# Kernel tuning notes

Hardware: AMD Instinct MI355X
Metric: run time of the kernel (lower is better)

The kernel has to match this reference:

```python
import jax, jax.numpy as jnp
import numpy as np

DIM = 3072
NUM_HEADS = 24
HEAD_DIM = 128
EPS = 1e-6


def setup_inputs() -> dict:
    key = jax.random.key(0)
    ks = jax.random.split(key, 16)
    B, S_new, S_cached = 2, 256, 8192
    s = 0.02
    return {
        "x": jax.random.normal(ks[0], (B, S_new, DIM), jnp.float32),
        "freqs": jax.random.uniform(ks[1], (S_new, HEAD_DIM // 2), jnp.float32, 0.0, 2 * np.pi),
        "k_cache": jax.random.normal(ks[2], (B, S_cached, DIM), jnp.float32),
        "v_cache": jax.random.normal(ks[3], (B, S_cached, DIM), jnp.float32),
        "Wq": jax.random.normal(ks[4], (DIM, DIM), jnp.float32) * s,
        "bq": jnp.zeros((DIM,), jnp.float32),
        "Wk": jax.random.normal(ks[5], (DIM, DIM), jnp.float32) * s,
        "bk": jnp.zeros((DIM,), jnp.float32),
        "Wv": jax.random.normal(ks[6], (DIM, DIM), jnp.float32) * s,
        "bv": jnp.zeros((DIM,), jnp.float32),
        "Wo": jax.random.normal(ks[7], (DIM, DIM), jnp.float32) * s,
        "bo": jnp.zeros((DIM,), jnp.float32),
        "gq": jnp.ones((DIM,), jnp.float32),
        "gk": jnp.ones((DIM,), jnp.float32),
    }


def _rmsnorm(t, g):
    return t * jax.lax.rsqrt(jnp.mean(t * t, axis=-1, keepdims=True) + EPS) * g


def _rope(t, freqs):
    # t: [B, S, DIM]; freqs: [S, HEAD_DIM//2] angles (complex e^{i*theta} multiply,
    # interleaved-pair layout, matching torch view_as_complex on (..., d//2, 2)).
    B, S, D = t.shape
    th = t.reshape(B, S, NUM_HEADS, HEAD_DIM // 2, 2)
    c = jnp.cos(freqs)[None, :, None, :]
    s = jnp.sin(freqs)[None, :, None, :]
    re = th[..., 0] * c - th[..., 1] * s
    im = th[..., 0] * s + th[..., 1] * c
    return jnp.stack([re, im], axis=-1).reshape(B, S, D)


def reference(x, freqs, k_cache, v_cache, Wq, bq, Wk, bk, Wv, bv, Wo, bo, gq, gk):
    B, S_new, _ = x.shape
    S_cached = k_cache.shape[1]
    S_tot = S_cached + S_new

    q = _rmsnorm(x @ Wq.T + bq, gq)
    k = _rmsnorm(x @ Wk.T + bk, gk)
    v = x @ Wv.T + bv

    q = _rope(q, freqs)
    k = _rope(k, freqs)

    # 'extend' cache mode: concat cached K/V with new K/V
    full_k = jnp.concatenate([k_cache, k], axis=1)
    full_v = jnp.concatenate([v_cache, v], axis=1)

    qh = q.reshape(B, S_new, NUM_HEADS, HEAD_DIM)
    kh = full_k.reshape(B, S_tot, NUM_HEADS, HEAD_DIM)
    vh = full_v.reshape(B, S_tot, NUM_HEADS, HEAD_DIM)

    scale = 1.0 / np.sqrt(HEAD_DIM)
    scores = jnp.einsum("bqhd,bkhd->bhqk", qh, kh) * scale
    probs = jax.nn.softmax(scores, axis=-1)
    out = jnp.einsum("bhqk,bkhd->bqhd", probs, vh).reshape(B, S_new, DIM)
    return out @ Wo.T + bo
```

## Files before the change

kernel.cpp:

```cpp
#include <hip/hip_runtime.h>
#include <hip/hip_bf16.h>

#define NH 24
#define HD 128
#define DM 3072
#define NB 2
#define SN 256
#define MR 512
#define SCACHE 8192
#define NCH 9

typedef float f32x4 __attribute__((ext_vector_type(4)));
typedef float f32x2 __attribute__((ext_vector_type(2)));
typedef short s16x8 __attribute__((ext_vector_type(8)));
typedef short s16x4 __attribute__((ext_vector_type(4)));
typedef unsigned u32x4 __attribute__((ext_vector_type(4)));

__device__ __forceinline__ short bfc(float f) {
    __hip_bfloat16 h = __float2bfloat16(f);
    return __builtin_bit_cast(short, h);
}

__global__ __launch_bounds__(256, 3) void gemm_bias(
    const float* __restrict__ A,
    const float* __restrict__ W0, const float* __restrict__ W1, const float* __restrict__ W2,
    const float* __restrict__ b0, const float* __restrict__ b1, const float* __restrict__ b2,
    float* __restrict__ O0, float* __restrict__ O1, float* __restrict__ O2)
{
    const int z = blockIdx.z;
    const float* W    = (z == 0) ? W0 : (z == 1) ? W1 : W2;
    const float* bias = (z == 0) ? b0 : (z == 1) ? b1 : b2;
    float* O          = (z == 0) ? O0 : (z == 1) ? O1 : O2;

    const int n0 = blockIdx.x * 128;
    const int m0 = blockIdx.y * 64;
    const int t = threadIdx.x;
    const int lane = t & 63;
    const int wave = t >> 6;
    const int l15 = lane & 15, l4 = lane >> 4;
    const int wm = (wave >> 1) * 32, wn = (wave & 1) * 64;

    __shared__ short As[64][72];
    __shared__ short Bs[128][72];

    f32x4 acc[2][4] = {};
    f32x4 areg[4], breg[8];

    #pragma unroll
    for (int i = 0; i < 4; ++i) {
        int lin = i * 256 + t;
        areg[i] = *(const f32x4*)(A + (size_t)(m0 + (lin >> 4)) * DM + (lin & 15) * 4);
    }
    #pragma unroll
    for (int i = 0; i < 8; ++i) {
        int lin = i * 256 + t;
        breg[i] = *(const f32x4*)(W + (size_t)(n0 + (lin >> 4)) * DM + (lin & 15) * 4);
    }

    for (int ks = 0; ks < DM / 64; ++ks) {
        #pragma unroll
        for (int i = 0; i < 4; ++i) {
            int lin = i * 256 + t;
            s16x4 a4;
            #pragma unroll
            for (int j = 0; j < 4; ++j) a4[j] = bfc(areg[i][j]);
            *(s16x4*)&As[lin >> 4][(lin & 15) * 4] = a4;
        }
        #pragma unroll
        for (int i = 0; i < 8; ++i) {
            int lin = i * 256 + t;
            s16x4 w4;
            #pragma unroll
            for (int j = 0; j < 4; ++j) w4[j] = bfc(breg[i][j]);
            *(s16x4*)&Bs[lin >> 4][(lin & 15) * 4] = w4;
        }
        __syncthreads();
        if (ks + 1 < DM / 64) {
            int k0 = (ks + 1) * 64;
            #pragma unroll
            for (int i = 0; i < 4; ++i) {
                int lin = i * 256 + t;
                areg[i] = *(const f32x4*)(A + (size_t)(m0 + (lin >> 4)) * DM + k0 + (lin & 15) * 4);
            }
            #pragma unroll
            for (int i = 0; i < 8; ++i) {
                int lin = i * 256 + t;
                breg[i] = *(const f32x4*)(W + (size_t)(n0 + (lin >> 4)) * DM + k0 + (lin & 15) * 4);
            }
        }
        #pragma unroll
        for (int kt = 0; kt < 2; ++kt) {
            s16x8 af[2], bfr[4];
            #pragma unroll
            for (int i = 0; i < 2; ++i)
                af[i]  = *(const s16x8*)&As[wm + i * 16 + l15][kt * 32 + l4 * 8];
            #pragma unroll
            for (int i = 0; i < 4; ++i)
                bfr[i] = *(const s16x8*)&Bs[wn + i * 16 + l15][kt * 32 + l4 * 8];
            #pragma unroll
            for (int mi = 0; mi < 2; ++mi)
                #pragma unroll
                for (int ni = 0; ni < 4; ++ni)
                    acc[mi][ni] = __builtin_amdgcn_mfma_f32_16x16x32_bf16(
                        af[mi], bfr[ni], acc[mi][ni], 0, 0, 0);
        }
        __syncthreads();
    }

    #pragma unroll
    for (int ni = 0; ni < 4; ++ni) {
        int col = n0 + wn + ni * 16 + l15;
        float bv = bias[col];
        #pragma unroll
        for (int mi = 0; mi < 2; ++mi) {
            int row = m0 + wm + mi * 16 + l4 * 4;
            #pragma unroll
            for (int r = 0; r < 4; ++r)
                O[(size_t)(row + r) * DM + col] = acc[mi][ni][r] + bv;
        }
    }
}

__global__ __launch_bounds__(256) void norm_rope(
    float* __restrict__ qf, float* __restrict__ kf, short* __restrict__ qbf,
    const float* __restrict__ gq, const float* __restrict__ gk,
    const float* __restrict__ freqs)
{
    const int buf = blockIdx.x >> 9;
    const int row = blockIdx.x & 511;
    const int t = threadIdx.x;
    float* src = buf ? kf : qf;
    const float* g = buf ? gk : gq;

    f32x2 v[6];
    float ss = 0.f;
    #pragma unroll
    for (int i = 0; i < 6; ++i) {
        int p = t + 256 * i;
        v[i] = *(const f32x2*)(src + (size_t)row * DM + 2 * p);
        ss += v[i][0] * v[i][0] + v[i][1] * v[i][1];
    }
    #pragma unroll
    for (int m = 1; m < 64; m <<= 1) ss += __shfl_xor(ss, m);
    __shared__ float red[4];
    if ((t & 63) == 0) red[t >> 6] = ss;
    __syncthreads();
    ss = red[0] + red[1] + red[2] + red[3];
    const float scale = rsqrtf(ss * (1.0f / DM) + 1e-6f);
    const float QS = 0.08838834764831845f * 1.4426950408889634f;

    const int spos = row & 255;
    #pragma unroll
    for (int i = 0; i < 6; ++i) {
        int p = t + 256 * i;
        int d2 = p & 63;
        float fr = freqs[spos * 64 + d2];
        float snv, cs;
        __sincosf(fr, &snv, &cs);
        f32x2 gg = *(const f32x2*)(g + 2 * p);
        float re = v[i][0] * scale * gg[0];
        float im = v[i][1] * scale * gg[1];
        float re2 = re * cs - im * snv;
        float im2 = re * snv + im * cs;
        if (buf == 0) {
            re2 *= QS; im2 *= QS;
            unsigned pack = (unsigned)(unsigned short)bfc(re2)
                          | ((unsigned)(unsigned short)bfc(im2) << 16);
            *(unsigned*)(qbf + (size_t)row * DM + 2 * p) = pack;
        } else {
            f32x2 o; o[0] = re2; o[1] = im2;
            *(f32x2*)(src + (size_t)row * DM + 2 * p) = o;
        }
    }
}

__global__ __launch_bounds__(512) void attn_fa(
    const short* __restrict__ qbf,
    const float* __restrict__ kf, const float* __restrict__ vf,
    const float* __restrict__ kcache, const float* __restrict__ vcache,
    float* __restrict__ partO, float* __restrict__ partM, float* __restrict__ partL)
{
    const int bid = blockIdx.x;
    const int linear = (bid & 7) * 54 + (bid >> 3);
    const int c  = linear / 48;
    const int bh = linear % 48;
    const int b = bh / NH, h = bh % NH;
    const int t = threadIdx.x, lane = t & 63, wave = t >> 6;
    const int l15 = lane & 15, l4 = lane >> 4;
    const int hoff = h * HD;

    __shared__ short KsA[2][64 * 128];
    __shared__ short VtA[2][128 * 64];

    s16x8 qb[2][4];
    #pragma unroll
    for (int nj = 0; nj < 2; ++nj) {
        int qrow = b * SN + wave * 32 + nj * 16 + l15;
        #pragma unroll
        for (int kt = 0; kt < 4; ++kt)
            qb[nj][kt] = *(const s16x8*)(qbf + (size_t)qrow * DM + hoff + kt * 32 + l4 * 8);
    }

    f32x4 acc[2][8] = {};
    float mrun[2] = {-INFINITY, -INFINITY};
    float lpart[2] = {0.f, 0.f};

    const int ts = (c < 6) ? c * 15 : 90 + (c - 6) * 14;
    const int NT = (c < 6) ? 15 : 14;

    const float* kcB = kcache + (size_t)b * SCACHE * DM + hoff;
    const float* knB = kf     + (size_t)b * SN * DM + hoff;
    const float* vcB = vcache + (size_t)b * SCACHE * DM + hoff;
    const float* vnB = vf     + (size_t)b * SN * DM + hoff;

    auto kaddr = [&](int r, int col) -> const float* {
        return (r < SCACHE) ? (kcB + (size_t)r * DM + col)
                            : (knB + (size_t)(r - SCACHE) * DM + col);
    };
    auto vaddr = [&](int r, int col) -> const float* {
        return (r < SCACHE) ? (vcB + (size_t)r * DM + col)
                            : (vnB + (size_t)(r - SCACHE) * DM + col);
    };

    const int vrow = t & 63, vw = t >> 6;
    f32x4 kreg[4], vreg[4];

    {
        const int kr = ts * 64;
        #pragma unroll
        for (int i = 0; i < 4; ++i) {
            int lin = i * 512 + t;
            kreg[i] = *(const f32x4*)kaddr(kr + (lin >> 5), (lin & 31) * 4);
        }
        #pragma unroll
        for (int j = 0; j < 4; ++j)
            vreg[j] = *(const f32x4*)vaddr(kr + vrow, vw * 16 + j * 4);
    }

    const bool ghi = (l4 & 2) != 0;
    const bool gin = (l4 == 0) || (l4 == 3);

    for (int nt = 0; nt < NT; ++nt) {
        char* KsB = (char*)KsA[nt & 1];
        char* VtB = (char*)VtA[nt & 1];

        #pragma unroll
        for (int i = 0; i < 4; ++i) {
            int lin = i * 512 + t;
            int row = lin >> 5, col4 = lin & 31;
            s16x4 k4;
            #pragma unroll
            for (int j = 0; j < 4; ++j) k4[j] = bfc(kreg[i][j]);
            *(s16x4*)(KsB + (row << 8) + ((((col4 >> 1) ^ row) & 15) << 4) + ((col4 & 1) << 3)) = k4;
        }
        #pragma unroll
        for (int j = 0; j < 4; ++j) {
            #pragma unroll
            for (int jj = 0; jj < 4; ++jj) {
                int d = vw * 16 + j * 4 + jj;
                *(short*)(VtB + (d << 7) + ((((vrow >> 3) ^ (d & 7))) << 4) + ((vrow & 7) << 1)) = bfc(vreg[j][jj]);
            }
        }
        __syncthreads();

        if (nt + 1 < NT) {
            const int kr1 = (ts + nt + 1) * 64;
            #pragma unroll
            for (int i = 0; i < 4; ++i) {
                int lin = i * 512 + t;
                kreg[i] = *(const f32x4*)kaddr(kr1 + (lin >> 5), (lin & 31) * 4);
            }
            #pragma unroll
            for (int j = 0; j < 4; ++j)
                vreg[j] = *(const f32x4*)vaddr(kr1 + vrow, vw * 16 + j * 4);
        }

        f32x4 st[4][2] = {};
        #pragma unroll
        for (int kt = 0; kt < 4; ++kt)
            #pragma unroll
            for (int mi = 0; mi < 4; ++mi) {
                int row = mi * 16 + l15;
                s16x8 kfr = *(const s16x8*)(KsB + (row << 8) + (((kt * 4 + l4) ^ l15) << 4));
                st[mi][0] = __builtin_amdgcn_mfma_f32_16x16x32_bf16(kfr, qb[0][kt], st[mi][0], 0, 0, 0);
                st[mi][1] = __builtin_amdgcn_mfma_f32_16x16x32_bf16(kfr, qb[1][kt], st[mi][1], 0, 0, 0);
            }

        float lx0 = fmaxf(
            fmaxf(fmaxf(fmaxf(st[0][0][0], st[0][0][1]), fmaxf(st[0][0][2], st[0][0][3])),
                  fmaxf(fmaxf(st[1][0][0], st[1][0][1]), fmaxf(st[1][0][2], st[1][0][3]))),
            fmaxf(fmaxf(fmaxf(st[2][0][0], st[2][0][1]), fmaxf(st[2][0][2], st[2][0][3])),
                  fmaxf(fmaxf(st[3][0][0], st[3][0][1]), fmaxf(st[3][0][2], st[3][0][3]))));
        float lx1 = fmaxf(
            fmaxf(fmaxf(fmaxf(st[0][1][0], st[0][1][1]), fmaxf(st[0][1][2], st[0][1][3])),
                  fmaxf(fmaxf(st[1][1][0], st[1][1][1]), fmaxf(st[1][1][2], st[1][1][3]))),
            fmaxf(fmaxf(fmaxf(st[2][1][0], st[2][1][1]), fmaxf(st[2][1][2], st[2][1][3])),
                  fmaxf(fmaxf(st[3][1][0], st[3][1][1]), fmaxf(st[3][1][2], st[3][1][3]))));

        if (!__all((lx0 <= mrun[0] + 8.0f) && (lx1 <= mrun[1] + 8.0f))) {
            float lm0 = fmaxf(lx0, __shfl_xor(lx0, 16)); lm0 = fmaxf(lm0, __shfl_xor(lm0, 32));
            float lm1 = fmaxf(lx1, __shfl_xor(lx1, 16)); lm1 = fmaxf(lm1, __shfl_xor(lm1, 32));
            float mn0 = fmaxf(mrun[0], lm0), mn1 = fmaxf(mrun[1], lm1);
            float c0 = exp2f(mrun[0] - mn0), c1 = exp2f(mrun[1] - mn1);
            mrun[0] = mn0; mrun[1] = mn1;
            lpart[0] *= c0; lpart[1] *= c1;
            #pragma unroll
            for (int df = 0; df < 8; ++df) { acc[0][df] *= c0; acc[1][df] *= c1; }
        }

        #pragma unroll
        for (int mi = 0; mi < 4; ++mi)
            #pragma unroll
            for (int r = 0; r < 4; ++r) {
                float p0 = exp2f(st[mi][0][r] - mrun[0]);
                float p1 = exp2f(st[mi][1][r] - mrun[1]);
                st[mi][0][r] = p0; st[mi][1][r] = p1;
                lpart[0] += p0; lpart[1] += p1;
            }

        unsigned up[2][4][2];
        #pragma unroll
        for (int nj = 0; nj < 2; ++nj)
            #pragma unroll
            for (int mi = 0; mi < 4; ++mi)
                #pragma unroll
                for (int i = 0; i < 2; ++i)
                    up[nj][mi][i] = (unsigned)(unsigned short)bfc(st[mi][nj][2 * i])
                                  | ((unsigned)(unsigned short)bfc(st[mi][nj][2 * i + 1]) << 16);

        s16x8 bp[2][2];
        #pragma unroll
        for (int nj = 0; nj < 2; ++nj)
            #pragma unroll
            for (int kt2 = 0; kt2 < 2; ++kt2) {
                unsigned own0 = ghi ? up[nj][kt2 * 2 + 1][0] : up[nj][kt2 * 2 + 0][0];
                unsigned own1 = ghi ? up[nj][kt2 * 2 + 1][1] : up[nj][kt2 * 2 + 0][1];
                unsigned alt0 = ghi ? up[nj][kt2 * 2 + 0][0] : up[nj][kt2 * 2 + 1][0];
                unsigned alt1 = ghi ? up[nj][kt2 * 2 + 0][1] : up[nj][kt2 * 2 + 1][1];
                unsigned o16_0 = __shfl_xor(own0, 16), o16_1 = __shfl_xor(own1, 16);
                unsigned o32_0 = __shfl_xor(alt0, 32), o32_1 = __shfl_xor(alt1, 32);
                unsigned o48_0 = __shfl_xor(alt0, 48), o48_1 = __shfl_xor(alt1, 48);
                u32x4 uu;
                uu[0] = gin ? (ghi ? o16_0 : own0) : (ghi ? o32_0 : o48_0);
                uu[1] = gin ? (ghi ? o16_1 : own1) : (ghi ? o32_1 : o48_1);
                uu[2] = gin ? (ghi ? own0 : o16_0) : (ghi ? o48_0 : o32_0);
                uu[3] = gin ? (ghi ? own1 : o16_1) : (ghi ? o48_1 : o32_1);
                bp[nj][kt2] = __builtin_bit_cast(s16x8, uu);
            }

        #pragma unroll
        for (int kt2 = 0; kt2 < 2; ++kt2)
            #pragma unroll
            for (int df = 0; df < 8; ++df) {
                int row = df * 16 + l15;
                s16x8 vfr = *(const s16x8*)(VtB + (row << 7) + (((kt2 * 4 + l4) ^ (row & 7)) << 4));
                acc[0][df] = __builtin_amdgcn_mfma_f32_16x16x32_bf16(vfr, bp[0][kt2], acc[0][df], 0, 0, 0);
                acc[1][df] = __builtin_amdgcn_mfma_f32_16x16x32_bf16(vfr, bp[1][kt2], acc[1][df], 0, 0, 0);
            }
    }

    float l0 = lpart[0]; l0 += __shfl_xor(l0, 16); l0 += __shfl_xor(l0, 32);
    float l1 = lpart[1]; l1 += __shfl_xor(l1, 16); l1 += __shfl_xor(l1, 32);

    #pragma unroll
    for (int nj = 0; nj < 2; ++nj) {
        size_t rowid = (size_t)bh * SN + wave * 32 + nj * 16 + l15;
        float* po = partO + (rowid * NCH + c) * HD + l4 * 4;
        #pragma unroll
        for (int df = 0; df < 8; ++df)
            *(f32x4*)(po + df * 16) = acc[nj][df];
        if (l4 == 0) {
            partM[rowid * NCH + c] = mrun[nj];
            partL[rowid * NCH + c] = (nj == 0) ? l0 : l1;
        }
    }
}

__global__ __launch_bounds__(128) void combine(
    const float* __restrict__ partO, const float* __restrict__ partM,
    const float* __restrict__ partL, float* __restrict__ attn)
{
    const int rowid = blockIdx.x;
    const int bh = rowid >> 8, q = rowid & 255;
    const int b = bh / NH, h = bh % NH;
    const int d = threadIdx.x;

    float m[NCH];
    float M = -INFINITY;
    #pragma unroll
    for (int c = 0; c < NCH; ++c) { m[c] = partM[(size_t)rowid * NCH + c]; M = fmaxf(M, m[c]); }
    float L = 0.f, o = 0.f;
    #pragma unroll
    for (int c = 0; c < NCH; ++c) {
        float w = exp2f(m[c] - M);
        L += partL[(size_t)rowid * NCH + c] * w;
        o += partO[((size_t)rowid * NCH + c) * HD + d] * w;
    }
    attn[(size_t)(b * SN + q) * DM + h * HD + d] = o / L;
}

extern "C" void kernel_launch(void* const* d_in, const int* in_sizes, int n_in,
                              void* d_out, int out_size, void* d_ws, size_t ws_size,
                              hipStream_t stream) {
    const float* x      = (const float*)d_in[0];
    const float* freqs  = (const float*)d_in[1];
    const float* kcache = (const float*)d_in[2];
    const float* vcache = (const float*)d_in[3];
    const float* Wq = (const float*)d_in[4];
    const float* bq = (const float*)d_in[5];
    const float* Wk = (const float*)d_in[6];
    const float* bk = (const float*)d_in[7];
    const float* Wv = (const float*)d_in[8];
    const float* bv = (const float*)d_in[9];
    const float* Wo = (const float*)d_in[10];
    const float* bo = (const float*)d_in[11];
    const float* gq = (const float*)d_in[12];
    const float* gk = (const float*)d_in[13];
    float* out = (float*)d_out;

    auto al = [](size_t v) { return (v + 255) & ~(size_t)255; };
    const size_t SZ_QF  = (size_t)MR * DM * 4;
    const size_t SZ_QBF = (size_t)MR * DM * 2;
    const size_t SZ_PML = (size_t)48 * SN * NCH * 4;
    const size_t SZ_PO  = (size_t)48 * SN * NCH * HD * 4;

    char* ws = (char*)d_ws;
    float* qf   = (float*)ws; ws += al(SZ_QF);
    float* kfb  = (float*)ws; ws += al(SZ_QF);
    float* vfb  = (float*)ws; ws += al(SZ_QF);
    short* qbf  = (short*)ws; ws += al(SZ_QBF);
    float* pM   = (float*)ws; ws += al(SZ_PML);
    float* pL   = (float*)ws; ws += al(SZ_PML);
    float* attn = (float*)ws; ws += al(SZ_QF);
    float* pO   = (float*)ws; ws += al(SZ_PO);

    gemm_bias<<<dim3(24, 8, 3), 256, 0, stream>>>(x, Wq, Wk, Wv, bq, bk, bv, qf, kfb, vfb);
    norm_rope<<<dim3(1024), 256, 0, stream>>>(qf, kfb, qbf, gq, gk, freqs);
    attn_fa<<<dim3(432), 512, 0, stream>>>(qbf, kfb, vfb, kcache, vcache, pO, pM, pL);
    combine<<<dim3(12288), 128, 0, stream>>>(pO, pM, pL, attn);
    gemm_bias<<<dim3(24, 8, 1), 256, 0, stream>>>(attn, Wo, Wo, Wo, bo, bo, bo, out, out, out);
}
```

Measured before the change: 312.4 us.

## Split KV into ten chunks, store partial outputs as bf16, pack V transpose stores

```diff
diff --git a/kernel.cpp b/kernel.cpp
--- a/kernel.cpp
+++ b/kernel.cpp
@@ -8,7 +8,7 @@
 #define SN 256
 #define MR 512
 #define SCACHE 8192
-#define NCH 9
+#define NCH 10
 
 typedef float f32x4 __attribute__((ext_vector_type(4)));
 typedef float f32x2 __attribute__((ext_vector_type(2)));
@@ -178,10 +178,10 @@
     const short* __restrict__ qbf,
     const float* __restrict__ kf, const float* __restrict__ vf,
     const float* __restrict__ kcache, const float* __restrict__ vcache,
-    float* __restrict__ partO, float* __restrict__ partM, float* __restrict__ partL)
+    short* __restrict__ partO, float* __restrict__ partM, float* __restrict__ partL)
 {
     const int bid = blockIdx.x;
-    const int linear = (bid & 7) * 54 + (bid >> 3);
+    const int linear = (bid & 7) * 60 + (bid >> 3);
     const int c  = linear / 48;
     const int bh = linear % 48;
     const int b = bh / NH, h = bh % NH;
@@ -205,36 +205,35 @@
     float mrun[2] = {-INFINITY, -INFINITY};
     float lpart[2] = {0.f, 0.f};
 
-    const int ts = (c < 6) ? c * 15 : 90 + (c - 6) * 14;
-    const int NT = (c < 6) ? 15 : 14;
+    const int ts = (c < 2) ? c * 14 : 28 + (c - 2) * 13;
+    const int NT = (c < 2) ? 14 : 13;
 
     const float* kcB = kcache + (size_t)b * SCACHE * DM + hoff;
     const float* knB = kf     + (size_t)b * SN * DM + hoff;
     const float* vcB = vcache + (size_t)b * SCACHE * DM + hoff;
     const float* vnB = vf     + (size_t)b * SN * DM + hoff;
 
-    auto kaddr = [&](int r, int col) -> const float* {
-        return (r < SCACHE) ? (kcB + (size_t)r * DM + col)
-                            : (knB + (size_t)(r - SCACHE) * DM + col);
+    auto bases = [&](int tile, const float*& kb_, const float*& vb_) {
+        int kr = tile * 64;
+        if (kr < SCACHE) { kb_ = kcB + (size_t)kr * DM; vb_ = vcB + (size_t)kr * DM; }
+        else { kb_ = knB + (size_t)(kr - SCACHE) * DM; vb_ = vnB + (size_t)(kr - SCACHE) * DM; }
     };
-    auto vaddr = [&](int r, int col) -> const float* {
-        return (r < SCACHE) ? (vcB + (size_t)r * DM + col)
-                            : (vnB + (size_t)(r - SCACHE) * DM + col);
-    };
-
-    const int vrow = t & 63, vw = t >> 6;
+
+    const int krow = t >> 5, kcol = (t & 31) * 4;
+    const int vk0 = (t & 31) * 2, vdb = (t >> 5) * 8;
     f32x4 kreg[4], vreg[4];
 
     {
-        const int kr = ts * 64;
-        #pragma unroll
-        for (int i = 0; i < 4; ++i) {
-            int lin = i * 512 + t;
-            kreg[i] = *(const f32x4*)kaddr(kr + (lin >> 5), (lin & 31) * 4);
-        }
-        #pragma unroll
-        for (int j = 0; j < 4; ++j)
-            vreg[j] = *(const f32x4*)vaddr(kr + vrow, vw * 16 + j * 4);
+        const float* kb; const float* vb;
+        bases(ts, kb, vb);
+        #pragma unroll
+        for (int i = 0; i < 4; ++i)
+            kreg[i] = *(const f32x4*)(kb + (size_t)(i * 16 + krow) * DM + kcol);
+        #pragma unroll
+        for (int j = 0; j < 2; ++j) {
+            vreg[j]     = *(const f32x4*)(vb + (size_t)vk0 * DM + vdb + j * 4);
+            vreg[2 + j] = *(const f32x4*)(vb + (size_t)(vk0 + 1) * DM + vdb + j * 4);
+        }
     }
 
     const bool ghi = (l4 & 2) != 0;
@@ -246,33 +245,32 @@
 
         #pragma unroll
         for (int i = 0; i < 4; ++i) {
-            int lin = i * 512 + t;
-            int row = lin >> 5, col4 = lin & 31;
+            int row = i * 16 + krow;
             s16x4 k4;
             #pragma unroll
             for (int j = 0; j < 4; ++j) k4[j] = bfc(kreg[i][j]);
-            *(s16x4*)(KsB + (row << 8) + ((((col4 >> 1) ^ row) & 15) << 4) + ((col4 & 1) << 3)) = k4;
-        }
-        #pragma unroll
-        for (int j = 0; j < 4; ++j) {
-            #pragma unroll
-            for (int jj = 0; jj < 4; ++jj) {
-                int d = vw * 16 + j * 4 + jj;
-                *(short*)(VtB + (d << 7) + ((((vrow >> 3) ^ (d & 7))) << 4) + ((vrow & 7) << 1)) = bfc(vreg[j][jj]);
-            }
+            *(s16x4*)(KsB + (row << 8) + ((((kcol >> 3) ^ row) & 15) << 4) + (((kcol >> 2) & 1) << 3)) = k4;
+        }
+        #pragma unroll
+        for (int jj = 0; jj < 8; ++jj) {
+            int d = vdb + jj;
+            unsigned pk = (unsigned)(unsigned short)bfc(vreg[jj >> 2][jj & 3])
+                        | ((unsigned)(unsigned short)bfc(vreg[2 + (jj >> 2)][jj & 3]) << 16);
+            *(unsigned*)(VtB + (d << 7) + ((((vk0 >> 3) ^ (d & 7))) << 4) + ((vk0 & 7) << 1)) = pk;
         }
         __syncthreads();
 
         if (nt + 1 < NT) {
-            const int kr1 = (ts + nt + 1) * 64;
-            #pragma unroll
-            for (int i = 0; i < 4; ++i) {
-                int lin = i * 512 + t;
-                kreg[i] = *(const f32x4*)kaddr(kr1 + (lin >> 5), (lin & 31) * 4);
-            }
-            #pragma unroll
-            for (int j = 0; j < 4; ++j)
-                vreg[j] = *(const f32x4*)vaddr(kr1 + vrow, vw * 16 + j * 4);
+            const float* kb; const float* vb;
+            bases(ts + nt + 1, kb, vb);
+            #pragma unroll
+            for (int i = 0; i < 4; ++i)
+                kreg[i] = *(const f32x4*)(kb + (size_t)(i * 16 + krow) * DM + kcol);
+            #pragma unroll
+            for (int j = 0; j < 2; ++j) {
+                vreg[j]     = *(const f32x4*)(vb + (size_t)vk0 * DM + vdb + j * 4);
+                vreg[2 + j] = *(const f32x4*)(vb + (size_t)(vk0 + 1) * DM + vdb + j * 4);
+            }
         }
 
         f32x4 st[4][2] = {};
@@ -365,10 +363,14 @@
     #pragma unroll
     for (int nj = 0; nj < 2; ++nj) {
         size_t rowid = (size_t)bh * SN + wave * 32 + nj * 16 + l15;
-        float* po = partO + (rowid * NCH + c) * HD + l4 * 4;
-        #pragma unroll
-        for (int df = 0; df < 8; ++df)
-            *(f32x4*)(po + df * 16) = acc[nj][df];
+        short* po = partO + (rowid * NCH + c) * HD + l4 * 4;
+        #pragma unroll
+        for (int df = 0; df < 8; ++df) {
+            s16x4 ob;
+            #pragma unroll
+            for (int r = 0; r < 4; ++r) ob[r] = bfc(acc[nj][df][r]);
+            *(s16x4*)(po + df * 16) = ob;
+        }
         if (l4 == 0) {
             partM[rowid * NCH + c] = mrun[nj];
             partL[rowid * NCH + c] = (nj == 0) ? l0 : l1;
@@ -377,7 +379,7 @@
 }
 
 __global__ __launch_bounds__(128) void combine(
-    const float* __restrict__ partO, const float* __restrict__ partM,
+    const short* __restrict__ partO, const float* __restrict__ partM,
     const float* __restrict__ partL, float* __restrict__ attn)
 {
     const int rowid = blockIdx.x;
@@ -394,7 +396,9 @@
     for (int c = 0; c < NCH; ++c) {
         float w = exp2f(m[c] - M);
         L += partL[(size_t)rowid * NCH + c] * w;
-        o += partO[((size_t)rowid * NCH + c) * HD + d] * w;
+        unsigned ub = (unsigned)(unsigned short)partO[((size_t)rowid * NCH + c) * HD + d];
+        float ov = __builtin_bit_cast(float, ub << 16);
+        o += ov * w;
     }
     attn[(size_t)(b * SN + q) * DM + h * HD + d] = o / L;
 }
@@ -422,7 +426,7 @@
     const size_t SZ_QF  = (size_t)MR * DM * 4;
     const size_t SZ_QBF = (size_t)MR * DM * 2;
     const size_t SZ_PML = (size_t)48 * SN * NCH * 4;
-    const size_t SZ_PO  = (size_t)48 * SN * NCH * HD * 4;
+    const size_t SZ_PO  = (size_t)48 * SN * NCH * HD * 2;
 
     char* ws = (char*)d_ws;
     float* qf   = (float*)ws; ws += al(SZ_QF);
@@ -432,11 +436,11 @@
     float* pM   = (float*)ws; ws += al(SZ_PML);
     float* pL   = (float*)ws; ws += al(SZ_PML);
     float* attn = (float*)ws; ws += al(SZ_QF);
-    float* pO   = (float*)ws; ws += al(SZ_PO);
+    short* pO   = (short*)ws; ws += al(SZ_PO);
 
     gemm_bias<<<dim3(24, 8, 3), 256, 0, stream>>>(x, Wq, Wk, Wv, bq, bk, bv, qf, kfb, vfb);
     norm_rope<<<dim3(1024), 256, 0, stream>>>(qf, kfb, qbf, gq, gk, freqs);
-    attn_fa<<<dim3(432), 512, 0, stream>>>(qbf, kfb, vfb, kcache, vcache, pO, pM, pL);
+    attn_fa<<<dim3(480), 512, 0, stream>>>(qbf, kfb, vfb, kcache, vcache, pO, pM, pL);
     combine<<<dim3(12288), 128, 0, stream>>>(pO, pM, pL, attn);
     gemm_bias<<<dim3(24, 8, 1), 256, 0, stream>>>(attn, Wo, Wo, Wo, bo, bo, bo, out, out, out);
 }
```

Measured after the change: 324.2 us. 1.04x slower.
